# Optimization experiments

Hardware: AMD Instinct MI355X
Metric: run time of the kernel (lower is better)

The kernel has to match this reference:

```python
import jax, jax.numpy as jnp
import numpy as np

HEADS = 8

def setup_inputs() -> dict:
    key = jax.random.key(0)
    ks = jax.random.split(key, 10)
    B, S, E = 2, 2048, 512
    q = jax.random.normal(ks[0], (B, S, E), jnp.float32)
    k = jax.random.normal(ks[1], (B, S, E), jnp.float32)
    v = jax.random.normal(ks[2], (B, S, E), jnp.float32)
    mask = jnp.zeros((S, S), jnp.float32)  # additive mask [s_q, s_k]
    scale = 0.02
    Wq = jax.random.normal(ks[3], (E, E), jnp.float32) * scale
    bq = jax.random.normal(ks[4], (E,), jnp.float32) * scale
    Wk = jax.random.normal(ks[5], (E, E), jnp.float32) * scale
    bk = jax.random.normal(ks[6], (E,), jnp.float32) * scale
    Wv = jax.random.normal(ks[7], (E, E), jnp.float32) * scale
    bv = jax.random.normal(ks[8], (E,), jnp.float32) * scale
    return {"q": q, "k": k, "v": v, "mask": mask,
            "Wq": Wq, "bq": bq, "Wk": Wk, "bk": bk, "Wv": Wv, "bv": bv}

def reference(q, k, v, mask, Wq, bq, Wk, bk, Wv, bv):
    H = HEADS
    b, s_q, _ = q.shape
    s_k = k.shape[1]
    s_v = v.shape[1]
    # NOTE: faithful to source: row-major view(b, H, s, -1) WITHOUT transposing
    # seq/head axes first (quirk of the original module).
    K = jnp.swapaxes((k @ Wk.T + bk).reshape(b, H, s_k, -1), 2, 3)  # [b,H,dh,s_k]
    Q = (q @ Wq.T + bq).reshape(b, H, s_q, -1)                      # [b,H,s_q,dh]
    V = (v @ Wv.T + bv).reshape(b, H, s_v, -1)                      # [b,H,s_v,dh]
    # NOTE: original scales by sqrt(K.shape[-1]) AFTER the transpose, i.e. sqrt(s_k)
    scores = (Q @ K) / jnp.sqrt(jnp.asarray(s_k, jnp.float32))      # [b,H,s_q,s_k]
    scores = scores + mask[:s_q, :s_k]
    attn = jax.nn.softmax(scores, axis=-1)
    out = (attn @ V).reshape(b, s_q, -1)  # [b, s_q, e]
    return out
```

## Files before the change

kernel.cpp:

```cpp
#include <hip/hip_runtime.h>


#define SEQ 2048
#define EMB 512
#define DH  64
#define MROWS 4096
#define NROWS 32768
#define L2E 1.4426950408889634f

typedef float  v4f __attribute__((ext_vector_type(4)));
typedef short  v8s __attribute__((ext_vector_type(8)));
typedef __fp16 v2h __attribute__((ext_vector_type(2)));

static __device__ __forceinline__ unsigned int f2bf(float f) {
    unsigned int u = __float_as_uint(f);
    u += 0x7fffu + ((u >> 16) & 1u);
    return u >> 16;
}
static __device__ __forceinline__ unsigned int pack2(float a, float b) {
    return f2bf(a) | (f2bf(b) << 16);
}
static __device__ __forceinline__ unsigned int cvtpk(float a, float b) {
    unsigned int r;
    asm("v_cvt_pk_bf16_f32 %0, %1, %2" : "=v"(r) : "v"(a), "v"(b));
    return r;
}
static __device__ __forceinline__ unsigned int packh2(float a, float b) {
    v2h h = __builtin_amdgcn_cvt_pkrtz(a, b);
    return __builtin_bit_cast(unsigned int, h);
}

__global__ __launch_bounds__(256, 3) void proj_kernel(
    const float* __restrict__ q, const float* __restrict__ k, const float* __restrict__ v,
    const float* __restrict__ Wq, const float* __restrict__ bq,
    const float* __restrict__ Wk, const float* __restrict__ bk,
    const float* __restrict__ Wv, const float* __restrict__ bv,
    const float* __restrict__ mask,
    unsigned short* __restrict__ Qbf, unsigned short* __restrict__ Kfr,
    unsigned short* __restrict__ Vbf, float* __restrict__ maskT,
    unsigned int* __restrict__ flags)
{
    __shared__ __align__(16) char smem[27648];
    const int tid = threadIdx.x;

    if (blockIdx.x >= 768) {
        const int mb2 = blockIdx.x - 768;
        const int rb = mb2 >> 5, kt = mb2 & 31;
        float* tile = maskT + ((size_t)rb * 32 + kt) * 8192;
        float4 vals[8];
        bool any = false;
#pragma unroll
        for (int i = 0; i < 8; ++i) {
            int s = tid + i * 256;
            int l  = s & 63;
            int cb = (s >> 6) & 3;
            int g  = (s >> 8) & 1;
            int w2 = (s >> 9) & 3;
            int qd2 = l >> 4, n2 = l & 15;
            vals[i] = *(const float4*)&mask[
                (size_t)(rb * 128 + w2 * 32 + g * 16 + n2) * SEQ + kt * 64 + cb * 16 + qd2 * 4];
            any = any | (vals[i].x != 0.f) | (vals[i].y != 0.f)
                      | (vals[i].z != 0.f) | (vals[i].w != 0.f);
        }
        unsigned int* nzp = (unsigned int*)smem;
        if (tid == 0) *nzp = 0u;
        __syncthreads();
        if (any) *nzp = 1u;
        __syncthreads();
        if (*nzp) {
#pragma unroll
            for (int i = 0; i < 8; ++i) {
                int s = tid + i * 256;
                vals[i].x *= L2E; vals[i].y *= L2E;
                vals[i].z *= L2E; vals[i].w *= L2E;
                *(float4*)&tile[(size_t)s * 4] = vals[i];
            }
            if (tid == 0) atomicOr(&flags[rb], 1u << kt);
        }
        return;
    }

    char* As = smem;
    char* Ws = smem + 9216;

    const int id  = blockIdx.x;
    const int pos = id & 31;
    const int nb  = pos >> 3;
    const int unit = (id >> 5) * 8 + (pos & 7);
    const int mb = unit & 63;
    const int z  = unit >> 6;

    const float* A    = (z == 0) ? q  : (z == 1) ? k  : v;
    const float* W    = (z == 0) ? Wq : (z == 1) ? Wk : Wv;
    const float* bias = (z == 0) ? bq : (z == 1) ? bk : bv;
    unsigned short* Cg = (z == 0) ? Qbf : Vbf;

    const int w    = tid >> 6;
    const int lane = tid & 63;
    const int qd   = lane >> 4;
    const int n    = lane & 15;
    const int m0 = mb * 64, n0 = nb * 128;

    float4 areg[4], wreg[8];
#pragma unroll
    for (int i = 0; i < 4; ++i) {
        int c = tid + i * 256;
        areg[i] = *(const float4*)&A[(size_t)(m0 + (c >> 4)) * EMB + (c & 15) * 4];
    }
#pragma unroll
    for (int i = 0; i < 8; ++i) {
        int c = tid + i * 256;
        wreg[i] = *(const float4*)&W[(size_t)(n0 + (c >> 4)) * EMB + (c & 15) * 4];
    }

    v4f acc[8];
#pragma unroll
    for (int cb = 0; cb < 8; ++cb) acc[cb] = (v4f)0.f;

#pragma unroll 1
    for (int kt = 0; kt < 8; ++kt) {
        __syncthreads();
#pragma unroll
        for (int i = 0; i < 4; ++i) {
            int c = tid + i * 256;
            uint2 pk = { cvtpk(areg[i].x, areg[i].y), cvtpk(areg[i].z, areg[i].w) };
            *(uint2*)&As[(c >> 4) * 144 + (c & 15) * 8] = pk;
        }
#pragma unroll
        for (int i = 0; i < 8; ++i) {
            int c = tid + i * 256;
            uint2 pk = { cvtpk(wreg[i].x, wreg[i].y), cvtpk(wreg[i].z, wreg[i].w) };
            *(uint2*)&Ws[(c >> 4) * 144 + (c & 15) * 8] = pk;
        }
        __syncthreads();

        if (kt + 1 < 8) {
#pragma unroll
            for (int i = 0; i < 4; ++i) {
                int c = tid + i * 256;
                areg[i] = *(const float4*)&A[(size_t)(m0 + (c >> 4)) * EMB + (kt+1) * 64 + (c & 15) * 4];
            }
#pragma unroll
            for (int i = 0; i < 8; ++i) {
                int c = tid + i * 256;
                wreg[i] = *(const float4*)&W[(size_t)(n0 + (c >> 4)) * EMB + (kt+1) * 64 + (c & 15) * 4];
            }
        }

#pragma unroll
        for (int ks = 0; ks < 2; ++ks) {
            v8s af = *(const v8s*)&As[(w * 16 + n) * 144 + ks * 64 + qd * 16];
#pragma unroll
            for (int cb = 0; cb < 8; ++cb) {
                v8s bfr = *(const v8s*)&Ws[(cb * 16 + n) * 144 + ks * 64 + qd * 16];
                acc[cb] = __builtin_amdgcn_mfma_f32_16x16x32_bf16(af, bfr, acc[cb], 0, 0, 0);
            }
        }
    }

    const float osc = (z == 0) ? 0.031879357905f : 1.0f;
    float bb[8];
#pragma unroll
    for (int cb = 0; cb < 8; ++cb) bb[cb] = bias[n0 + cb * 16 + n];
#pragma unroll
    for (int cb = 0; cb < 8; ++cb)
#pragma unroll
        for (int r = 0; r < 4; ++r) acc[cb][r] = (acc[cb][r] + bb[cb]) * osc;

    __syncthreads();
    short* Ct = (short*)smem;
#pragma unroll
    for (int cb = 0; cb < 8; ++cb)
#pragma unroll
        for (int r = 0; r < 2; ++r) {
            unsigned int pk = cvtpk(acc[cb][2*r], acc[cb][2*r+1]);
            Ct[(w * 16 + qd * 4 + 2*r)     * 136 + cb * 16 + n] = (short)(pk & 0xffffu);
            Ct[(w * 16 + qd * 4 + 2*r + 1) * 136 + cb * 16 + n] = (short)(pk >> 16);
        }
    __syncthreads();
    const int rr = tid >> 2, q4 = tid & 3;
    if (z == 1) {
        const int bh = m0 >> 8;
        const int mm = (m0 & 255) + rr;
        unsigned short* Kh = Kfr + (size_t)bh * 32 * 4096;
#pragma unroll
        for (int i = 0; i < 4; ++i) {
            uint4 t4 = *(const uint4*)&smem[rr * 272 + q4 * 64 + i * 16];
            int nn = n0 + q4 * 32 + i * 8;
            int s  = mm * 8 + (nn >> 6);
            int kt = s >> 6, sk = s & 63;
            int dd = nn & 63;
            int entry = ((dd >> 5) * 4 + (sk >> 4)) * 64 + ((dd & 31) >> 3) * 16 + (sk & 15);
            *(uint4*)&Kh[(size_t)kt * 4096 + entry * 8] = t4;
        }
    } else {
#pragma unroll
        for (int i = 0; i < 4; ++i) {
            uint4 t4 = *(const uint4*)&smem[rr * 272 + q4 * 64 + i * 16];
            *(uint4*)&Cg[(size_t)(m0 + rr) * EMB + n0 + q4 * 32 + i * 8] = t4;
        }
    }
}

__global__ __launch_bounds__(256) void frag_kernel(
    const unsigned short* __restrict__ Vbf, unsigned short* __restrict__ Vfr)
{
    __shared__ unsigned short T[64 * 136];
    const int bh = blockIdx.x, kt = blockIdx.y;
    const int tid = threadIdx.x;

    const unsigned short* Vh = Vbf + (size_t)bh * (SEQ * DH) + (size_t)kt * 64 * DH;
#pragma unroll
    for (int i = 0; i < 2; ++i) {
        int c = tid + i * 256;
        int s_l = c >> 3, ch = c & 7;
        uint4 t4 = *(const uint4*)&Vh[c * 8];
        const unsigned short* e = (const unsigned short*)&t4;
#pragma unroll
        for (int j = 0; j < 8; ++j)
            T[(ch * 8 + j) * 136 + s_l] = e[j];
    }
    __syncthreads();
    unsigned short* Vo = Vfr + ((size_t)bh * 32 + kt) * 4096;
#pragma unroll
    for (int i = 0; i < 2; ++i) {
        int idx = tid + i * 256;
        int f = idx >> 6, l = idx & 63;
        int ks = f >> 2, cb = f & 3, qd = l >> 4, n = l & 15;
        uint4 t4 = *(const uint4*)&T[(cb * 16 + n) * 136 + ks * 32 + qd * 8];
        *(uint4*)&Vo[idx * 8] = t4;
    }
}

template <int SPLITS>
__global__ __launch_bounds__(256, 6) void attn_kernel(
    const unsigned short* __restrict__ Qbf,
    const unsigned short* __restrict__ Kfr, const unsigned short* __restrict__ Vfr,
    const float* __restrict__ maskT, const float* __restrict__ maskf,
    const unsigned int* __restrict__ flags,
    unsigned short* __restrict__ Opart, float* __restrict__ ml,
    float* __restrict__ out)
{
    __shared__ __align__(16) char smem[17408];
    const int tid  = threadIdx.x;
    const int w    = tid >> 6;
    const int lane = tid & 63;
    const int qd   = lane >> 4;
    const int n    = lane & 15;
    const int a_   = qd & 1;
    const bool diag = (a_ == (qd >> 1));

    const int id = blockIdx.x;
    const int bh = (id & 7) * 2 + ((id >> 3) & 1);
    const int unit = id >> 4;
    const int rb6 = unit & 31;
    const int kq = unit >> 5;
    const int KT0 = kq * (32 / SPLITS), KT1 = KT0 + 32 / SPLITS;

    const unsigned short* Qh  = Qbf + (size_t)bh * (SEQ * DH);
    const unsigned short* Kfh = Kfr + (size_t)bh * 32 * 4096;
    const unsigned short* Vfh = Vfr + (size_t)bh * 32 * 4096;

    const unsigned int fl = (SPLITS > 1) ? flags[rb6 >> 1] : 0u;

    v8s qf[2];
    {
        const size_t qrow = (size_t)(rb6 * 64 + w * 16 + n);
#pragma unroll
        for (int ks = 0; ks < 2; ++ks)
            qf[ks] = *(const v8s*)&Qh[qrow * DH + ks * 32 + qd * 8];
    }

    float l_ = 0.f;
    v4f oacc[4];
#pragma unroll
    for (int cb = 0; cb < 4; ++cb) oacc[cb] = (v4f)0.f;

#pragma unroll 1
    for (int kt = KT0; kt < KT1; ++kt) {
        const unsigned short* Kt = Kfh + (size_t)kt * 4096;
        const unsigned short* Vt = Vfh + (size_t)kt * 4096;

        v4f sacc[4];
        float4 mk[4];
        if (SPLITS > 1) {
            if (fl & (1u << kt)) {
                const float* tileF = maskT + ((size_t)(rb6 >> 1) * 32 + kt) * 8192;
                const int wg = (rb6 & 1) * 4 + w;
#pragma unroll
                for (int cb = 0; cb < 4; ++cb)
                    sacc[cb] = *(const v4f*)&tileF[
                        (size_t)((wg * 4 + cb) * 64 + qd * 16 + n) * 4];
            } else {
#pragma unroll
                for (int cb = 0; cb < 4; ++cb) sacc[cb] = (v4f)0.f;
            }
        } else {
            const size_t mrow = (size_t)(rb6 * 64 + w * 16 + n);
#pragma unroll
            for (int cb = 0; cb < 4; ++cb) {
                mk[cb] = *(const float4*)&maskf[mrow * SEQ + kt * 64 + cb * 16 + qd * 4];
                sacc[cb] = (v4f)0.f;
            }
        }

#pragma unroll
        for (int ks = 0; ks < 2; ++ks)
#pragma unroll
            for (int cb = 0; cb < 4; ++cb) {
                v8s kf = *(const v8s*)&Kt[((ks * 4 + cb) * 64 + lane) * 8];
                sacc[cb] = __builtin_amdgcn_mfma_f32_16x16x32_bf16(kf, qf[ks], sacc[cb], 0, 0, 0);
            }

        v8s pfr[2];
        {
            float rs = 0.f;
            unsigned int O_[4][2];
#pragma unroll
            for (int cb = 0; cb < 4; ++cb) {
                float s0 = sacc[cb][0], s1 = sacc[cb][1];
                float s2 = sacc[cb][2], s3 = sacc[cb][3];
                if (SPLITS == 1) {
                    s0 = fmaf(mk[cb].x, L2E, s0);
                    s1 = fmaf(mk[cb].y, L2E, s1);
                    s2 = fmaf(mk[cb].z, L2E, s2);
                    s3 = fmaf(mk[cb].w, L2E, s3);
                }
                float e0 = __builtin_amdgcn_exp2f(s0);
                float e1 = __builtin_amdgcn_exp2f(s1);
                float e2 = __builtin_amdgcn_exp2f(s2);
                float e3 = __builtin_amdgcn_exp2f(s3);
                rs += (e0 + e1) + (e2 + e3);
                O_[cb][0] = pack2(e0, e1);
                O_[cb][1] = pack2(e2, e3);
            }
            rs += __shfl_xor(rs, 16);
            rs += __shfl_xor(rs, 32);
            l_ += rs;
#pragma unroll
            for (int ks = 0; ks < 2; ++ks) {
                unsigned int t0 = a_ ? O_[2 * ks][0] : O_[2 * ks + 1][0];
                unsigned int t1 = a_ ? O_[2 * ks][1] : O_[2 * ks + 1][1];
                unsigned int r0 = __shfl_xor(t0, 16);
                unsigned int r1 = __shfl_xor(t1, 16);
                unsigned int Z00 = a_ ? r0 : O_[2 * ks][0];
                unsigned int Z01 = a_ ? r1 : O_[2 * ks][1];
                unsigned int Z10 = a_ ? O_[2 * ks + 1][0] : r0;
                unsigned int Z11 = a_ ? O_[2 * ks + 1][1] : r1;
                unsigned int s00 = __shfl_xor(Z00, 48);
                unsigned int s01 = __shfl_xor(Z01, 48);
                unsigned int s10 = __shfl_xor(Z10, 48);
                unsigned int s11 = __shfl_xor(Z11, 48);
                uint4 pw;
                pw.x = diag ? Z00 : s00;
                pw.y = diag ? Z01 : s01;
                pw.z = diag ? Z10 : s10;
                pw.w = diag ? Z11 : s11;
                pfr[ks] = __builtin_bit_cast(v8s, pw);
            }
        }

#pragma unroll
        for (int ks = 0; ks < 2; ++ks)
#pragma unroll
            for (int cb = 0; cb < 4; ++cb) {
                v8s vf = *(const v8s*)&Vt[((ks * 4 + cb) * 64 + lane) * 8];
                oacc[cb] = __builtin_amdgcn_mfma_f32_16x16x32_bf16(vf, pfr[ks], oacc[cb], 0, 0, 0);
            }
    }

    if (SPLITS == 1) {
        const float inv = 1.0f / l_;
#pragma unroll
        for (int cb = 0; cb < 4; ++cb)
#pragma unroll
            for (int r = 0; r < 4; ++r) oacc[cb][r] *= inv;
    } else {
        if (qd == 0) {
            const size_t row = (size_t)bh * SEQ + rb6 * 64 + w * 16 + n;
            ml[(size_t)kq * NROWS + row] = l_;
        }
    }
    __syncthreads();
#pragma unroll
    for (int cb = 0; cb < 4; ++cb)
        *(v4f*)&smem[(w * 16 + n) * 272 + cb * 64 + qd * 16] = oacc[cb];
    __syncthreads();
    const int r_l = tid >> 2, q4 = tid & 3;
    if (SPLITS == 1) {
        float* dst = &out[((size_t)bh * SEQ + rb6 * 64 + r_l) * DH + q4 * 16];
#pragma unroll
        for (int i = 0; i < 4; ++i) {
            float4 t4 = *(const float4*)&smem[r_l * 272 + q4 * 64 + i * 16];
            *(float4*)&dst[i * 4] = t4;
        }
    } else {
        unsigned short* dst = &Opart[((size_t)kq * NROWS + (size_t)bh * SEQ + rb6 * 64 + r_l) * DH + q4 * 16];
#pragma unroll
        for (int i = 0; i < 2; ++i) {
            float4 f0 = *(const float4*)&smem[r_l * 272 + q4 * 64 + i * 32];
            float4 f1 = *(const float4*)&smem[r_l * 272 + q4 * 64 + i * 32 + 16];
            uint4 o = { packh2(f0.x, f0.y), packh2(f0.z, f0.w),
                        packh2(f1.x, f1.y), packh2(f1.z, f1.w) };
            *(uint4*)&dst[i * 8] = o;
        }
    }
}

__global__ __launch_bounds__(256) void combine_kernel(
    const unsigned int* __restrict__ Opart, const float* __restrict__ ml,
    float* __restrict__ out, int splits)
{
    const int tid = threadIdx.x;
    const size_t row = (size_t)blockIdx.x * 16 + (tid >> 4);
    const int d4 = (tid & 15) * 4;
    float denom = 0.f;
    float4 o = make_float4(0.f, 0.f, 0.f, 0.f);
    for (int s = 0; s < splits; ++s) {
        denom += ml[(size_t)s * NROWS + row];
        uint2 u = *(const uint2*)&Opart[((size_t)s * NROWS + row) * 32 + (d4 >> 1)];
        v2h h0 = __builtin_bit_cast(v2h, u.x);
        v2h h1 = __builtin_bit_cast(v2h, u.y);
        o.x += (float)h0.x; o.y += (float)h0.y;
        o.z += (float)h1.x; o.w += (float)h1.y;
    }
    const float inv = 1.0f / denom;
    o.x *= inv; o.y *= inv; o.z *= inv; o.w *= inv;
    *(float4*)&out[row * DH + d4] = o;
}

extern "C" void kernel_launch(void* const* d_in, const int* in_sizes, int n_in,
                              void* d_out, int out_size, void* d_ws, size_t ws_size,
                              hipStream_t stream) {
    const float* q    = (const float*)d_in[0];
    const float* k    = (const float*)d_in[1];
    const float* v    = (const float*)d_in[2];
    const float* mask = (const float*)d_in[3];
    const float* Wq   = (const float*)d_in[4];
    const float* bq   = (const float*)d_in[5];
    const float* Wk   = (const float*)d_in[6];
    const float* bk   = (const float*)d_in[7];
    const float* Wv   = (const float*)d_in[8];
    const float* bv   = (const float*)d_in[9];

    char* ws = (char*)d_ws;
    const size_t MB = 1024 * 1024;
    unsigned short* Qbf   = (unsigned short*)(ws + 0);
    unsigned short* Kbf   = (unsigned short*)(ws + 4 * MB);
    unsigned short* Vfr   = (unsigned short*)(ws + 8 * MB);
    unsigned short* Opart = (unsigned short*)(ws + 12 * MB);
    unsigned short* Vbf   = (unsigned short*)(ws + 12 * MB);
    float*          mlp   = (float*)(ws + 28 * MB);
    unsigned int*   flags = (unsigned int*)(ws + 28 * MB + 512 * 1024);
    float*          maskT = (float*)(ws + 29 * MB);
    (void)Kbf;

    const size_t need_split = 49 * MB;
    const bool do_split = ws_size >= need_split;

    if (do_split) {
        unsigned short* Kfr = (unsigned short*)(ws + 45 * MB);
        (void)hipMemsetAsync(flags, 0, 64, stream);
        proj_kernel<<<1280, 256, 0, stream>>>(q, k, v, Wq, bq, Wk, bk, Wv, bv,
                                              mask, Qbf, Kfr, Vbf, maskT, flags);
        dim3 tgrid(16, 32);
        frag_kernel<<<tgrid, 256, 0, stream>>>(Vbf, Vfr);
        attn_kernel<4><<<2048, 256, 0, stream>>>(Qbf, Kfr, Vfr, maskT, mask, flags,
                                                 Opart, mlp, (float*)d_out);
        combine_kernel<<<NROWS / 16, 256, 0, stream>>>((const unsigned int*)Opart,
                                                       mlp, (float*)d_out, 4);
    } else {
        unsigned short* Kfr = (unsigned short*)(ws + 16 * MB);
        proj_kernel<<<768, 256, 0, stream>>>(q, k, v, Wq, bq, Wk, bk, Wv, bv,
                                             mask, Qbf, Kfr, Vbf, maskT, flags);
        dim3 tgrid(16, 32);
        frag_kernel<<<tgrid, 256, 0, stream>>>(Vbf, Vfr);
        attn_kernel<1><<<512, 256, 0, stream>>>(Qbf, Kfr, Vfr, maskT, mask, flags,
                                                Opart, mlp, (float*)d_out);
    }
}
```

Baseline: 171.0 us.

## Fuse split-K combine into attention via last-block atomic counter; drop memset

Removes the separate combine kernel: each attention block increments a per-(head,row-block) counter after writing its partial, and the fourth arriving block reduces the four partials and writes the final output. The mask-nonzero flags become per-tile words written directly rather than atomically OR'd, so the hipMemsetAsync launch is dropped, and the counters are zeroed inside frag_kernel. This saves two launches and a pass over the partials, at the cost of threadfences, an atomic per block, and serialized tail work in the last block.

Measured after the change: 447.7 us. 162% more time.

```diff
diff --git a/kernel.cpp b/kernel.cpp
--- a/kernel.cpp
+++ b/kernel.cpp
@@ -38,7 +38,7 @@
     const float* __restrict__ mask,
     unsigned short* __restrict__ Qbf, unsigned short* __restrict__ Kfr,
     unsigned short* __restrict__ Vbf, float* __restrict__ maskT,
-    unsigned int* __restrict__ flags)
+    unsigned int* __restrict__ flagw)
 {
     __shared__ __align__(16) char smem[27648];
     const int tid = threadIdx.x;
@@ -67,6 +67,7 @@
         __syncthreads();
         if (any) *nzp = 1u;
         __syncthreads();
+        if (tid == 0) flagw[rb * 32 + kt] = *nzp;
         if (*nzp) {
 #pragma unroll
             for (int i = 0; i < 8; ++i) {
@@ -75,7 +76,6 @@
                 vals[i].z *= L2E; vals[i].w *= L2E;
                 *(float4*)&tile[(size_t)s * 4] = vals[i];
             }
-            if (tid == 0) atomicOr(&flags[rb], 1u << kt);
         }
         return;
     }
@@ -203,11 +203,13 @@
 }
 
 __global__ __launch_bounds__(256) void frag_kernel(
-    const unsigned short* __restrict__ Vbf, unsigned short* __restrict__ Vfr)
+    const unsigned short* __restrict__ Vbf, unsigned short* __restrict__ Vfr,
+    unsigned int* __restrict__ cnt)
 {
     __shared__ unsigned short T[64 * 136];
     const int bh = blockIdx.x, kt = blockIdx.y;
     const int tid = threadIdx.x;
+    if (tid == 0) cnt[bh * 32 + kt] = 0u;
 
     const unsigned short* Vh = Vbf + (size_t)bh * (SEQ * DH) + (size_t)kt * 64 * DH;
 #pragma unroll
@@ -237,11 +239,12 @@
     const unsigned short* __restrict__ Qbf,
     const unsigned short* __restrict__ Kfr, const unsigned short* __restrict__ Vfr,
     const float* __restrict__ maskT, const float* __restrict__ maskf,
-    const unsigned int* __restrict__ flags,
+    const unsigned int* __restrict__ flagw, unsigned int* __restrict__ cnt,
     unsigned short* __restrict__ Opart, float* __restrict__ ml,
     float* __restrict__ out)
 {
     __shared__ __align__(16) char smem[17408];
+    __shared__ unsigned int lastf;
     const int tid  = threadIdx.x;
     const int w    = tid >> 6;
     const int lane = tid & 63;
@@ -260,8 +263,7 @@
     const unsigned short* Qh  = Qbf + (size_t)bh * (SEQ * DH);
     const unsigned short* Kfh = Kfr + (size_t)bh * 32 * 4096;
     const unsigned short* Vfh = Vfr + (size_t)bh * 32 * 4096;
-
-    const unsigned int fl = (SPLITS > 1) ? flags[rb6 >> 1] : 0u;
+    const unsigned int* fwb = flagw + (rb6 >> 1) * 32;
 
     v8s qf[2];
     {
@@ -284,7 +286,7 @@
         v4f sacc[4];
         float4 mk[4];
         if (SPLITS > 1) {
-            if (fl & (1u << kt)) {
+            if (fwb[kt] != 0u) {
                 const float* tileF = maskT + ((size_t)(rb6 >> 1) * 32 + kt) * 8192;
                 const int wg = (rb6 & 1) * 4 + w;
 #pragma unroll
@@ -404,29 +406,40 @@
                         packh2(f1.x, f1.y), packh2(f1.z, f1.w) };
             *(uint4*)&dst[i * 8] = o;
         }
-    }
-}
-
-__global__ __launch_bounds__(256) void combine_kernel(
-    const unsigned int* __restrict__ Opart, const float* __restrict__ ml,
-    float* __restrict__ out, int splits)
-{
-    const int tid = threadIdx.x;
-    const size_t row = (size_t)blockIdx.x * 16 + (tid >> 4);
-    const int d4 = (tid & 15) * 4;
-    float denom = 0.f;
-    float4 o = make_float4(0.f, 0.f, 0.f, 0.f);
-    for (int s = 0; s < splits; ++s) {
-        denom += ml[(size_t)s * NROWS + row];
-        uint2 u = *(const uint2*)&Opart[((size_t)s * NROWS + row) * 32 + (d4 >> 1)];
-        v2h h0 = __builtin_bit_cast(v2h, u.x);
-        v2h h1 = __builtin_bit_cast(v2h, u.y);
-        o.x += (float)h0.x; o.y += (float)h0.y;
-        o.z += (float)h1.x; o.w += (float)h1.y;
-    }
-    const float inv = 1.0f / denom;
-    o.x *= inv; o.y *= inv; o.z *= inv; o.w *= inv;
-    *(float4*)&out[row * DH + d4] = o;
+
+        __threadfence();
+        __syncthreads();
+        if (tid == 0)
+            lastf = (atomicAdd(&cnt[bh * 32 + rb6], 1u) == 3u) ? 1u : 0u;
+        __syncthreads();
+        if (lastf) {
+            __threadfence();
+            const int d0 = (tid & 3) * 16;
+            const size_t row = (size_t)bh * SEQ + rb6 * 64 + r_l;
+            float denom = 0.f;
+            float a[16];
+#pragma unroll
+            for (int i = 0; i < 16; ++i) a[i] = 0.f;
+#pragma unroll 1
+            for (int s = 0; s < 4; ++s) {
+                denom += ml[(size_t)s * NROWS + row];
+                const uint2* op = (const uint2*)&Opart[((size_t)s * NROWS + row) * DH + d0];
+#pragma unroll
+                for (int j = 0; j < 4; ++j) {
+                    uint2 u = op[j];
+                    v2h h0 = __builtin_bit_cast(v2h, u.x);
+                    v2h h1 = __builtin_bit_cast(v2h, u.y);
+                    a[j*4+0] += (float)h0.x; a[j*4+1] += (float)h0.y;
+                    a[j*4+2] += (float)h1.x; a[j*4+3] += (float)h1.y;
+                }
+            }
+            const float inv = 1.0f / denom;
+            float4* dstf = (float4*)&out[row * DH + d0];
+#pragma unroll
+            for (int j = 0; j < 4; ++j)
+                dstf[j] = make_float4(a[j*4]*inv, a[j*4+1]*inv, a[j*4+2]*inv, a[j*4+3]*inv);
+        }
+    }
 }
 
 extern "C" void kernel_launch(void* const* d_in, const int* in_sizes, int n_in,
@@ -446,36 +459,32 @@
     char* ws = (char*)d_ws;
     const size_t MB = 1024 * 1024;
     unsigned short* Qbf   = (unsigned short*)(ws + 0);
-    unsigned short* Kbf   = (unsigned short*)(ws + 4 * MB);
     unsigned short* Vfr   = (unsigned short*)(ws + 8 * MB);
     unsigned short* Opart = (unsigned short*)(ws + 12 * MB);
     unsigned short* Vbf   = (unsigned short*)(ws + 12 * MB);
     float*          mlp   = (float*)(ws + 28 * MB);
-    unsigned int*   flags = (unsigned int*)(ws + 28 * MB + 512 * 1024);
+    unsigned int*   flagw = (unsigned int*)(ws + 28 * MB + 512 * 1024);
+    unsigned int*   cnt   = (unsigned int*)(ws + 28 * MB + 520 * 1024);
     float*          maskT = (float*)(ws + 29 * MB);
-    (void)Kbf;
 
     const size_t need_split = 49 * MB;
     const bool do_split = ws_size >= need_split;
 
     if (do_split) {
         unsigned short* Kfr = (unsigned short*)(ws + 45 * MB);
-        (void)hipMemsetAsync(flags, 0, 64, stream);
         proj_kernel<<<1280, 256, 0, stream>>>(q, k, v, Wq, bq, Wk, bk, Wv, bv,
-                                              mask, Qbf, Kfr, Vbf, maskT, flags);
+                                              mask, Qbf, Kfr, Vbf, maskT, flagw);
         dim3 tgrid(16, 32);
-        frag_kernel<<<tgrid, 256, 0, stream>>>(Vbf, Vfr);
-        attn_kernel<4><<<2048, 256, 0, stream>>>(Qbf, Kfr, Vfr, maskT, mask, flags,
-                                                 Opart, mlp, (float*)d_out);
-        combine_kernel<<<NROWS / 16, 256, 0, stream>>>((const unsigned int*)Opart,
-                                                       mlp, (float*)d_out, 4);
+        frag_kernel<<<tgrid, 256, 0, stream>>>(Vbf, Vfr, cnt);
+        attn_kernel<4><<<2048, 256, 0, stream>>>(Qbf, Kfr, Vfr, maskT, mask, flagw,
+                                                 cnt, Opart, mlp, (float*)d_out);
     } else {
         unsigned short* Kfr = (unsigned short*)(ws + 16 * MB);
         proj_kernel<<<768, 256, 0, stream>>>(q, k, v, Wq, bq, Wk, bk, Wv, bv,
-                                             mask, Qbf, Kfr, Vbf, maskT, flags);
+                                             mask, Qbf, Kfr, Vbf, maskT, flagw);
         dim3 tgrid(16, 32);
-        frag_kernel<<<tgrid, 256, 0, stream>>>(Vbf, Vfr);
-        attn_kernel<1><<<512, 256, 0, stream>>>(Qbf, Kfr, Vfr, maskT, mask, flags,
-                                                Opart, mlp, (float*)d_out);
-    }
-}
+        frag_kernel<<<tgrid, 256, 0, stream>>>(Vbf, Vfr, cnt);
+        attn_kernel<1><<<512, 256, 0, stream>>>(Qbf, Kfr, Vfr, maskT, mask, flagw,
+                                                cnt, Opart, mlp, (float*)d_out);
+    }
+}
```
